# Kernel optimization log

Hardware: AMD Instinct MI355X
Metric: run time of the kernel (lower is better)

The kernel has to match this reference:

```python
import jax, jax.numpy as jnp
import numpy as np

N = 100000   # nodes
E = 1600000  # edges
B = 4096     # graphs
F_IN = 92
H = 51       # hidden_channels
ED = 10      # edge_dim
T = 7        # num_timesteps

def _p(key, shape, scale=0.1):
    return scale * jax.random.normal(key, shape, dtype=jnp.float32)

def setup_inputs():
    key = jax.random.key(0)
    ks = jax.random.split(key, 20)
    return {
        "x": jax.random.normal(ks[0], (N, F_IN), dtype=jnp.float32),
        "edge_index": jax.random.randint(ks[1], (2, E), 0, N),
        "edge_attr": jax.random.normal(ks[2], (E, ED), dtype=jnp.float32),
        "batch": jnp.sort(jax.random.randint(ks[3], (N,), 0, B)),
        "W1": _p(ks[4], (F_IN, H)), "b1": jnp.zeros((H,), jnp.float32),
        "We1": _p(ks[5], (H + ED, H)),
        "att_l": _p(ks[6], (H,)), "att_r": _p(ks[7], (H,)),
        "We2": _p(ks[8], (H, H)), "gate_bias": jnp.zeros((H,), jnp.float32),
        "Wih1": _p(ks[9], (H, 3 * H)), "bih1": jnp.zeros((3 * H,), jnp.float32),
        "Whh1": _p(ks[10], (H, 3 * H)), "bhh1": jnp.zeros((3 * H,), jnp.float32),
        "Wm": _p(ks[11], (H, H)),
        "att_src": _p(ks[12], (H,)), "att_dst": _p(ks[13], (H,)),
        "mol_bias": jnp.zeros((H,), jnp.float32),
        "Wih2": _p(ks[14], (H, 3 * H)), "bih2": jnp.zeros((3 * H,), jnp.float32),
        "Whh2": _p(ks[15], (H, 3 * H)), "bhh2": jnp.zeros((3 * H,), jnp.float32),
        "W2": _p(ks[16], (H, 1)), "b2": jnp.zeros((1,), jnp.float32),
    }

def _lrelu(v):
    return jax.nn.leaky_relu(v, 0.01)

def _seg_softmax(a, idx, num):
    # scatter-softmax over segments (PyG softmax with 1e-16 denom eps)
    m = jax.ops.segment_max(a, idx, num_segments=num)
    e = jnp.exp(a - m[idx])
    s = jax.ops.segment_sum(e, idx, num_segments=num)
    return e / (s[idx] + 1e-16)

def _gru(xin, h, Wih, bih, Whh, bhh):
    # torch.nn.GRUCell, gate order r, z, n
    gi = xin @ Wih + bih
    gh = h @ Whh + bhh
    ir, iz, inn = jnp.split(gi, 3, axis=-1)
    hr, hz, hn = jnp.split(gh, 3, axis=-1)
    r = jax.nn.sigmoid(ir + hr)
    z = jax.nn.sigmoid(iz + hz)
    n = jnp.tanh(inn + r * hn)
    return (1.0 - z) * n + z * h

def reference(x, edge_index, edge_attr, batch, W1, b1, We1, att_l, att_r, We2,
              gate_bias, Wih1, bih1, Whh1, bhh1, Wm, att_src, att_dst, mol_bias,
              Wih2, bih2, Whh2, bhh2, W2, b2):
    src, dst = edge_index[0], edge_index[1]
    # AttentiveFP.lin1 + leaky_relu
    x = _lrelu(x @ W1 + b1)                                        # (N, H)
    # GATEConv: edge-conditioned attention, aggregate to dst
    xe = _lrelu(jnp.concatenate([x[src], edge_attr], axis=-1) @ We1)  # (E, H)
    a = _lrelu(xe @ att_l + x[dst] @ att_r)                        # (E,)
    alpha = _seg_softmax(a, dst, N)
    h = jax.ops.segment_sum((xe @ We2) * alpha[:, None], dst, num_segments=N) + gate_bias
    h = jax.nn.elu(h)                                              # dropout off (eval)
    x = jax.nn.relu(_gru(h, x, Wih1, bih1, Whh1, bhh1))            # (N, H)
    # molecule readout: GATConv over bipartite (nodes -> graphs) edges (arange(N), batch)
    out = jax.nn.relu(jax.ops.segment_sum(x, batch, num_segments=B))  # (B, H)
    xl = x @ Wm                                                    # (N, H), constant over t
    al = xl @ att_src                                              # (N,)
    for _ in range(T):
        ar = (out @ Wm) @ att_dst                                  # (B,)
        a = _lrelu(al + ar[batch])
        alpha = _seg_softmax(a, batch, B)
        hm = jax.ops.segment_sum(xl * alpha[:, None], batch, num_segments=B) + mol_bias
        hm = jax.nn.elu(hm)
        out = jax.nn.relu(_gru(hm, out, Wih2, bih2, Whh2, bhh2))
    return out @ W2 + b2                                           # (B, 1)
```

## Files before the change

kernel.cpp:

```cpp
#include <hip/hip_runtime.h>
#include <stdint.h>

#define NN 100000
#define NE 1600000
#define NB 4096
#define FIN 92
#define H 51
#define H3 153
#define TSTEPS 7
#define SCAN_B 391
#define GG_BLOCKS 1024
#define GG_CHUNKS (NN / 32)

__device__ __align__(16) float g_x1[(size_t)NN * 52 + 64];
__device__ __align__(16) float g_p[(size_t)NN * 52 + 64];
__device__ float g_xr[NN];
__device__ float g_agg[(size_t)NN * H + 64];
__device__ float g_x2[(size_t)NN * H + 64];
__device__ float g_xl[(size_t)NN * H + 64];
__device__ float g_al[NN];
__device__ int   g_gs[NB + 2];
__device__ float g_wg1[H * H * 8];
__device__ float g_bg1[64 * 8];
__device__ float g_wg2[H * H * 8];
__device__ float g_bg2[64 * 8];
__device__ float g_wv[64];
__device__ int   g_cnt[NN];
__device__ int   g_rp[NN + 1];
__device__ int   g_cur[NN];
__device__ int   g_src[NE + 4];
__device__ __align__(16) float g_eac[(size_t)NE * 12 + 16];
__device__ int   g_bsum[512];
__device__ int   g_boff[512];

__device__ __forceinline__ float lrelu(float v) { return v > 0.f ? v : 0.01f * v; }
__device__ __forceinline__ float elu1(float v) { return v > 0.f ? v : expm1f(v); }
__device__ __forceinline__ float sigm(float v) { return 1.f / (1.f + __expf(-v)); }

__device__ __forceinline__ float bflo(uint32_t w) { union { uint32_t u; float f; } c; c.u = w << 16; return c.f; }
__device__ __forceinline__ float bfhi(uint32_t w) { union { uint32_t u; float f; } c; c.u = w & 0xffff0000u; return c.f; }
__device__ __forceinline__ uint32_t f2bf(float f) {
    uint32_t u = __float_as_uint(f);
    return (u + 0x7FFFu + ((u >> 16) & 1u)) >> 16;
}

__device__ __forceinline__ float wave_sum(float v) {
    v += __shfl_xor(v, 32, 64);
    v += __shfl_xor(v, 16, 64);
    v += __shfl_xor(v, 8, 64);
    v += __shfl_xor(v, 4, 64);
    v += __shfl_xor(v, 2, 64);
    v += __shfl_xor(v, 1, 64);
    return v;
}
__device__ __forceinline__ void wave_sum4(float& a, float& b, float& c, float& d) {
    a += __shfl_xor(a, 32, 64); b += __shfl_xor(b, 32, 64); c += __shfl_xor(c, 32, 64); d += __shfl_xor(d, 32, 64);
    a += __shfl_xor(a, 16, 64); b += __shfl_xor(b, 16, 64); c += __shfl_xor(c, 16, 64); d += __shfl_xor(d, 16, 64);
    a += __shfl_xor(a, 8, 64);  b += __shfl_xor(b, 8, 64);  c += __shfl_xor(c, 8, 64);  d += __shfl_xor(d, 8, 64);
    a += __shfl_xor(a, 4, 64);  b += __shfl_xor(b, 4, 64);  c += __shfl_xor(c, 4, 64);  d += __shfl_xor(d, 4, 64);
    a += __shfl_xor(a, 2, 64);  b += __shfl_xor(b, 2, 64);  c += __shfl_xor(c, 2, 64);  d += __shfl_xor(d, 2, 64);
    a += __shfl_xor(a, 1, 64);  b += __shfl_xor(b, 1, 64);  c += __shfl_xor(c, 1, 64);  d += __shfl_xor(d, 1, 64);
}

__device__ __forceinline__ float d4(float acc, float4 t, float4 wv) {
    return fmaf(t.x, wv.x, fmaf(t.y, wv.y, fmaf(t.z, wv.z, fmaf(t.w, wv.w, acc))));
}

__global__ __launch_bounds__(256) void k_init(const int* __restrict__ batch) {
    int n = blockIdx.x * 256 + threadIdx.x;
    if (n >= NN) return;
    g_cnt[n] = 0;
    int bn = batch[n];
    int bp = (n == 0) ? -1 : batch[n - 1];
    for (int b = bp + 1; b <= bn; ++b) g_gs[b] = n;
    if (n == NN - 1) for (int b = bn + 1; b <= NB; ++b) g_gs[b] = NN;
}

__global__ void k_prep(const float* __restrict__ Wih1, const float* __restrict__ bih1,
                       const float* __restrict__ Whh1, const float* __restrict__ bhh1,
                       const float* __restrict__ Wih2, const float* __restrict__ bih2,
                       const float* __restrict__ Whh2, const float* __restrict__ bhh2,
                       const float* __restrict__ Wm, const float* __restrict__ ad) {
    int id = blockIdx.x * 256 + threadIdx.x;
    int which = 0;
    const float *Wih, *bih, *Whh, *bhh;
    if (id < H * H) {
        which = 0; Wih = Wih1; bih = bih1; Whh = Whh1; bhh = bhh1;
    } else if (id < 2 * H * H) {
        which = 1; id -= H * H; Wih = Wih2; bih = bih2; Whh = Whh2; bhh = bhh2;
    } else {
        int k = id - 2 * H * H;
        if (k < 64) {
            float a = 0.f;
            if (k < H) for (int j = 0; j < H; ++j) a = fmaf(Wm[k * H + j], ad[j], a);
            g_wv[k] = a;
        }
        return;
    }
    float* Wg = which ? g_wg2 : g_wg1;
    float* bg = which ? g_bg2 : g_bg1;
    int k = id / H, j = id - k * H;
    float* o = Wg + (size_t)id * 8;
    o[0] = Wih[k * H3 + j];
    o[1] = Wih[k * H3 + H + j];
    o[2] = Wih[k * H3 + 2 * H + j];
    o[3] = Whh[k * H3 + j];
    o[4] = Whh[k * H3 + H + j];
    o[5] = Whh[k * H3 + 2 * H + j];
    o[6] = 0.f; o[7] = 0.f;
    if (id < H) {
        float* ob = bg + (size_t)id * 8;
        ob[0] = bih[id]; ob[1] = bih[H + id]; ob[2] = bih[2 * H + id];
        ob[3] = bhh[id]; ob[4] = bhh[H + id]; ob[5] = bhh[2 * H + id];
        ob[6] = 0.f; ob[7] = 0.f;
    }
}

__global__ __launch_bounds__(256) void k_count(const int* __restrict__ ei) {
    int e = blockIdx.x * 256 + threadIdx.x;
    if (e >= NE) return;
    atomicAdd(&g_cnt[ei[NE + e]], 1);
}

__global__ __launch_bounds__(256) void k_scan1() {
    __shared__ int sm[256];
    int tid = threadIdx.x;
    int i = blockIdx.x * 256 + tid;
    sm[tid] = (i < NN) ? g_cnt[i] : 0;
    __syncthreads();
#pragma unroll
    for (int off = 1; off < 256; off <<= 1) {
        int t = (tid >= off) ? sm[tid - off] : 0;
        __syncthreads();
        sm[tid] += t;
        __syncthreads();
    }
    if (i < NN) g_rp[i + 1] = sm[tid];
    if (tid == 255) g_bsum[blockIdx.x] = sm[255];
}

__global__ void k_scan2() {
    __shared__ int sm[512];
    int tid = threadIdx.x;
    sm[tid] = (tid < SCAN_B) ? g_bsum[tid] : 0;
    __syncthreads();
#pragma unroll
    for (int off = 1; off < 512; off <<= 1) {
        int t = (tid >= off) ? sm[tid - off] : 0;
        __syncthreads();
        sm[tid] += t;
        __syncthreads();
    }
    if (tid < SCAN_B) g_boff[tid] = (tid == 0) ? 0 : sm[tid - 1];
}

__global__ __launch_bounds__(256) void k_scan3() {
    int i = blockIdx.x * 256 + threadIdx.x;
    if (i >= NN) return;
    int v = g_rp[i + 1] + g_boff[blockIdx.x];
    g_rp[i + 1] = v;
    if (i == 0) { g_rp[0] = 0; g_cur[0] = 0; }
    if (i + 1 < NN) g_cur[i + 1] = v;
}

__global__ __launch_bounds__(256) void k_fill(const int* __restrict__ ei, const float* __restrict__ ea) {
    int e = blockIdx.x * 256 + threadIdx.x;
    if (e >= NE) return;
    int d = ei[NE + e];
    int pos = atomicAdd(&g_cur[d], 1);
    g_src[pos] = ei[e];
    const float2* s2 = (const float2*)(ea + (size_t)e * 10);
    float2 v0 = s2[0], v1 = s2[1], v2 = s2[2], v3 = s2[3], v4 = s2[4];
    float2* d2 = (float2*)(g_eac + (size_t)pos * 12);
    d2[0] = v0; d2[1] = v1; d2[2] = v2; d2[3] = v3; d2[4] = v4;
    d2[5] = make_float2(0.f, 0.f);
}

__global__ __launch_bounds__(256, 3) void k_lin1(const float* __restrict__ x, const float* __restrict__ W1,
                                                 const float* __restrict__ b1, const float* __restrict__ attr_,
                                                 const float* __restrict__ We1) {
    int n = blockIdx.x * 256 + threadIdx.x;
    if (n >= NN) return;
    const float4* xq4 = (const float4*)(x + (size_t)n * FIN);
    float acc[H];
#pragma unroll
    for (int h = 0; h < H; ++h) acc[h] = 0.f;
#pragma unroll 1
    for (int q = 0; q < FIN / 4; ++q) {
        float4 v = xq4[q];
        const float* wr = W1 + (4 * q) * H;
#pragma unroll
        for (int h = 0; h < H; ++h)
            acc[h] = fmaf(v.x, wr[h], fmaf(v.y, wr[H + h], fmaf(v.z, wr[2 * H + h], fmaf(v.w, wr[3 * H + h], acc[h]))));
    }
    float xrv = 0.f;
    float* xo = g_x1 + (size_t)n * 52;
#pragma unroll
    for (int h = 0; h < H; ++h) {
        float v = lrelu(acc[h] + b1[h]);
        acc[h] = v;
        xo[h] = v;
        xrv = fmaf(v, attr_[h], xrv);
    }
    xo[H] = 0.f;
    g_xr[n] = xrv;
    float* po = g_p + (size_t)n * 52;
#pragma unroll 1
    for (int h = 0; h < H; ++h) {
        float ph = 0.f;
#pragma unroll
        for (int k = 0; k < H; ++k) ph = fmaf(acc[k], We1[k * H + h], ph);
        po[h] = ph;
    }
    po[H] = 0.f;
}

#define MKE(q) make_float4( \
    (4*(q)+0) < 10 ? We1[(51 + 4*(q)+0) * H + lj] : 0.f, \
    (4*(q)+1) < 10 ? We1[(51 + 4*(q)+1) * H + lj] : 0.f, \
    (4*(q)+2) < 10 ? We1[(51 + 4*(q)+2) * H + lj] : 0.f, \
    (4*(q)+3) < 10 ? We1[(51 + 4*(q)+3) * H + lj] : 0.f)

__global__ __launch_bounds__(256, 4) void k_gate(const float* __restrict__ We1, const float* __restrict__ attl) {
    int lane = threadIdx.x & 63;
    int lj = lane < H ? lane : H - 1;
    int n = __builtin_amdgcn_readfirstlane(blockIdx.x * 4 + (threadIdx.x >> 6));
    float4 eq0 = MKE(0), eq1 = MKE(1), eq2 = MKE(2);
    float attlv = attl[lj];
    float xrd = g_xr[n];
    int rs = g_rp[n], re = g_rp[n + 1];
    float accH = 0.f, den = 0.f;
    int nb = (re - rs) >> 2;
    int idx = rs;
    float pv0 = 0.f, pv1 = 0.f, pv2 = 0.f, pv3 = 0.f;
    if (nb > 0) {
        int s0 = __builtin_amdgcn_readfirstlane(g_src[idx]);
        int s1 = __builtin_amdgcn_readfirstlane(g_src[idx + 1]);
        int s2 = __builtin_amdgcn_readfirstlane(g_src[idx + 2]);
        int s3 = __builtin_amdgcn_readfirstlane(g_src[idx + 3]);
        pv0 = g_p[(size_t)s0 * 52 + lane];
        pv1 = g_p[(size_t)s1 * 52 + lane];
        pv2 = g_p[(size_t)s2 * 52 + lane];
        pv3 = g_p[(size_t)s3 * 52 + lane];
    }
#pragma unroll 1
    for (int blk = 0; blk < nb; ++blk) {
        int ci = idx;
        float cp0 = pv0, cp1 = pv1, cp2 = pv2, cp3 = pv3;
        idx += 4;
        if (blk + 1 < nb) {
            int s0 = __builtin_amdgcn_readfirstlane(g_src[idx]);
            int s1 = __builtin_amdgcn_readfirstlane(g_src[idx + 1]);
            int s2 = __builtin_amdgcn_readfirstlane(g_src[idx + 2]);
            int s3 = __builtin_amdgcn_readfirstlane(g_src[idx + 3]);
            pv0 = g_p[(size_t)s0 * 52 + lane];
            pv1 = g_p[(size_t)s1 * 52 + lane];
            pv2 = g_p[(size_t)s2 * 52 + lane];
            pv3 = g_p[(size_t)s3 * 52 + lane];
        }
        const float4* ep0 = (const float4*)(g_eac + (size_t)ci * 12);
        const float4* ep1 = (const float4*)(g_eac + (size_t)(ci + 1) * 12);
        const float4* ep2 = (const float4*)(g_eac + (size_t)(ci + 2) * 12);
        const float4* ep3 = (const float4*)(g_eac + (size_t)(ci + 3) * 12);
        float xe0 = cp0, xe1 = cp1, xe2 = cp2, xe3 = cp3;
        xe0 = d4(xe0, ep0[0], eq0); xe0 = d4(xe0, ep0[1], eq1); xe0 = d4(xe0, ep0[2], eq2);
        xe1 = d4(xe1, ep1[0], eq0); xe1 = d4(xe1, ep1[1], eq1); xe1 = d4(xe1, ep1[2], eq2);
        xe2 = d4(xe2, ep2[0], eq0); xe2 = d4(xe2, ep2[1], eq1); xe2 = d4(xe2, ep2[2], eq2);
        xe3 = d4(xe3, ep3[0], eq0); xe3 = d4(xe3, ep3[1], eq1); xe3 = d4(xe3, ep3[2], eq2);
        float l0 = lrelu(xe0), l1 = lrelu(xe1), l2 = lrelu(xe2), l3 = lrelu(xe3);
        float p0 = (lane < H) ? l0 * attlv : 0.f;
        float p1 = (lane < H) ? l1 * attlv : 0.f;
        float p2 = (lane < H) ? l2 * attlv : 0.f;
        float p3 = (lane < H) ? l3 * attlv : 0.f;
        wave_sum4(p0, p1, p2, p3);
        float e0 = __expf(lrelu(p0 + xrd));
        float e1 = __expf(lrelu(p1 + xrd));
        float e2 = __expf(lrelu(p2 + xrd));
        float e3 = __expf(lrelu(p3 + xrd));
        accH = fmaf(e0, l0, accH); den += e0;
        accH = fmaf(e1, l1, accH); den += e1;
        accH = fmaf(e2, l2, accH); den += e2;
        accH = fmaf(e3, l3, accH); den += e3;
    }
    for (; idx < re; ++idx) {
        int s0 = __builtin_amdgcn_readfirstlane(g_src[idx]);
        float pvs = g_p[(size_t)s0 * 52 + lane];
        const float4* ep0 = (const float4*)(g_eac + (size_t)idx * 12);
        float xe0 = pvs;
        xe0 = d4(xe0, ep0[0], eq0); xe0 = d4(xe0, ep0[1], eq1); xe0 = d4(xe0, ep0[2], eq2);
        float l0 = lrelu(xe0);
        float a0 = wave_sum((lane < H) ? l0 * attlv : 0.f);
        float e0 = __expf(lrelu(a0 + xrd));
        accH = fmaf(e0, l0, accH); den += e0;
    }
    if (lane < H) g_agg[(size_t)n * H + lane] = accH / (den + 1e-16f);
}

__global__ __launch_bounds__(256) void k_gategru(const float* __restrict__ We2, const float* __restrict__ gb,
                                                 const float* __restrict__ Wm, const float* __restrict__ asrc) {
    __shared__ uint32_t wA[H * H];
    __shared__ uint32_t wB[H * H];
    __shared__ uint32_t wC[H * H];
    __shared__ float lbc[4][52][8];
    int tid = threadIdx.x;
    for (int i = tid; i < H * H; i += 256) {
        const float* s = g_wg1 + (size_t)i * 8;
        wA[i] = f2bf(s[0]) | (f2bf(s[1]) << 16);
        wB[i] = f2bf(s[2]) | (f2bf(s[3]) << 16);
        wC[i] = f2bf(s[4]) | (f2bf(s[5]) << 16);
    }
    __syncthreads();
    int w = tid >> 6;
    int lane = tid & 63;
    int lj = lane < H ? lane : H - 1;
    const float4* bp = (const float4*)(g_bg1 + lane * 8);
    float4 b0 = bp[0];
    float4 b1v = bp[1];
    float gbl = gb[lj];
    float asl = asrc[lj];
#pragma unroll 1
    for (int chunk = blockIdx.x; chunk < GG_CHUNKS; chunk += GG_BLOCKS) {
        int base = __builtin_amdgcn_readfirstlane(chunk * 32 + w * 8);
        float xj[8];
#pragma unroll
        for (int m = 0; m < 8; ++m) xj[m] = g_x1[(size_t)(base + m) * 52 + lane];
        float ac[8];
#pragma unroll
        for (int m = 0; m < 8; ++m) ac[m] = 0.f;
#pragma unroll 1
        for (int k = 0; k < H; ++k) {
            float wv = We2[k * H + lj];
#pragma unroll
            for (int m = 0; m < 8; ++m)
                ac[m] = fmaf(g_agg[(size_t)(base + m) * H + k], wv, ac[m]);
        }
        float hb[8];
#pragma unroll
        for (int m = 0; m < 8; ++m) hb[m] = elu1(ac[m] + gbl);
        if (lane < H) {
#pragma unroll
            for (int m = 0; m < 8; ++m) lbc[w][lane][m] = hb[m];
        }
        float gir[8], giz[8], gin[8], ghr[8], ghz[8], ghn[8];
#pragma unroll
        for (int m = 0; m < 8; ++m) { gir[m] = 0; giz[m] = 0; gin[m] = 0; ghr[m] = 0; ghz[m] = 0; ghn[m] = 0; }
#pragma unroll 1
        for (int k = 0; k < H; ++k) {
            uint32_t wa = wA[k * H + lj];
            uint32_t wb = wB[k * H + lj];
            uint32_t wc = wC[k * H + lj];
            float w0x = bflo(wa), w0y = bfhi(wa), w0z = bflo(wb);
            float w0w = bfhi(wb), w1x = bflo(wc), w1y = bfhi(wc);
            float4 h0 = *(const float4*)&lbc[w][k][0];
            float4 h1 = *(const float4*)&lbc[w][k][4];
            float hk[8] = { h0.x, h0.y, h0.z, h0.w, h1.x, h1.y, h1.z, h1.w };
#pragma unroll
            for (int m = 0; m < 8; ++m) {
                float xk = g_x1[(size_t)(base + m) * 52 + k];
                gir[m] = fmaf(hk[m], w0x, gir[m]); giz[m] = fmaf(hk[m], w0y, giz[m]); gin[m] = fmaf(hk[m], w0z, gin[m]);
                ghr[m] = fmaf(xk, w0w, ghr[m]);    ghz[m] = fmaf(xk, w1x, ghz[m]);    ghn[m] = fmaf(xk, w1y, ghn[m]);
            }
        }
        float o2[8];
#pragma unroll
        for (int m = 0; m < 8; ++m) {
            float r = sigm(gir[m] + b0.x + ghr[m] + b0.w);
            float z = sigm(giz[m] + b0.y + ghz[m] + b1v.x);
            float nn2 = tanhf(gin[m] + b0.z + r * (ghn[m] + b1v.y));
            o2[m] = fmaxf((1.f - z) * nn2 + z * xj[m], 0.f);
            if (lane < H) g_x2[(size_t)(base + m) * H + lane] = o2[m];
        }
        if (lane < H) {
#pragma unroll
            for (int m = 0; m < 8; ++m) lbc[w][lane][m] = o2[m];
        }
        float xl[8];
#pragma unroll
        for (int m = 0; m < 8; ++m) xl[m] = 0.f;
#pragma unroll 1
        for (int k = 0; k < H; ++k) {
            float wv = Wm[k * H + lj];
            float4 o0 = *(const float4*)&lbc[w][k][0];
            float4 o1 = *(const float4*)&lbc[w][k][4];
            xl[0] = fmaf(o0.x, wv, xl[0]); xl[1] = fmaf(o0.y, wv, xl[1]);
            xl[2] = fmaf(o0.z, wv, xl[2]); xl[3] = fmaf(o0.w, wv, xl[3]);
            xl[4] = fmaf(o1.x, wv, xl[4]); xl[5] = fmaf(o1.y, wv, xl[5]);
            xl[6] = fmaf(o1.z, wv, xl[6]); xl[7] = fmaf(o1.w, wv, xl[7]);
        }
        float v0, v1, v2, v3, v4, v5, v6, v7;
        v0 = (lane < H) ? xl[0] * asl : 0.f;
        v1 = (lane < H) ? xl[1] * asl : 0.f;
        v2 = (lane < H) ? xl[2] * asl : 0.f;
        v3 = (lane < H) ? xl[3] * asl : 0.f;
        v4 = (lane < H) ? xl[4] * asl : 0.f;
        v5 = (lane < H) ? xl[5] * asl : 0.f;
        v6 = (lane < H) ? xl[6] * asl : 0.f;
        v7 = (lane < H) ? xl[7] * asl : 0.f;
        wave_sum4(v0, v1, v2, v3);
        wave_sum4(v4, v5, v6, v7);
#pragma unroll
        for (int m = 0; m < 8; ++m)
            if (lane < H) g_xl[(size_t)(base + m) * H + lane] = xl[m];
        if (lane == 0) {
            g_al[base + 0] = v0; g_al[base + 1] = v1; g_al[base + 2] = v2; g_al[base + 3] = v3;
            g_al[base + 4] = v4; g_al[base + 5] = v5; g_al[base + 6] = v6; g_al[base + 7] = v7;
        }
    }
}

__global__ __launch_bounds__(256) void k_mol_all(const float* __restrict__ mb, const float* __restrict__ W2,
                                                 const float* __restrict__ b2, float* __restrict__ dout) {
    __shared__ uint32_t ldsWa[H * H];
    __shared__ uint32_t ldsWb[H * H];
    __shared__ uint32_t ldsWc[H * H];
    __shared__ float lbc[4][52][2];
    int tid = threadIdx.x;
    for (int i = tid; i < H * H; i += 256) {
        const float* s = g_wg2 + (size_t)i * 8;
        ldsWa[i] = f2bf(s[0]) | (f2bf(s[1]) << 16);
        ldsWb[i] = f2bf(s[2]) | (f2bf(s[3]) << 16);
        ldsWc[i] = f2bf(s[4]) | (f2bf(s[5]) << 16);
    }
    __syncthreads();
    int w = tid >> 6;
    int lane = tid & 63;
    int lj = lane < H ? lane : H - 1;
    int b = __builtin_amdgcn_readfirstlane(blockIdx.x * 4 + w);
    int gs = g_gs[b], ge = g_gs[b + 1];
    float oa = 0.f, ob = 0.f;
    int i = gs;
    for (; i + 2 <= ge; i += 2) {
        oa += g_x2[(size_t)i * H + lane];
        ob += g_x2[(size_t)(i + 1) * H + lane];
    }
    if (i < ge) oa += g_x2[(size_t)i * H + lane];
    float oj = fmaxf(oa + ob, 0.f);
    float wvl = g_wv[lane];
    float mbl = mb[lj];
    const float4* bp = (const float4*)(g_bg2 + lane * 8);
    float4 b0 = bp[0];
    float4 b1v = bp[1];
#pragma unroll 1
    for (int t = 0; t < TSTEPS; ++t) {
        float arb = wave_sum((lane < H) ? oj * wvl : 0.f);
        float sa = 0.f, sb = 0.f, aa = 0.f, ab = 0.f;
        i = gs;
        for (; i + 2 <= ge; i += 2) {
            float ev0 = __expf(lrelu(g_al[i] + arb));
            float ev1 = __expf(lrelu(g_al[i + 1] + arb));
            sa += ev0; sb += ev1;
            aa = fmaf(ev0, g_xl[(size_t)i * H + lane], aa);
            ab = fmaf(ev1, g_xl[(size_t)(i + 1) * H + lane], ab);
        }
        if (i < ge) {
            float ev0 = __expf(lrelu(g_al[i] + arb));
            sa += ev0;
            aa = fmaf(ev0, g_xl[(size_t)i * H + lane], aa);
        }
        float inv = 1.f / (sa + sb + 1e-16f);
        float hm = elu1((aa + ab) * inv + mbl);
        if (lane < H) { lbc[w][lane][0] = hm; lbc[w][lane][1] = oj; }
        float gir = 0, giz = 0, gin = 0, ghr = 0, ghz = 0, ghn = 0;
#pragma unroll 2
        for (int k = 0; k < H; ++k) {
            uint32_t wa = ldsWa[k * H + lj];
            uint32_t wb = ldsWb[k * H + lj];
            uint32_t wc = ldsWc[k * H + lj];
            float2 ho = *(const float2*)&lbc[w][k][0];
            float hmk = ho.x, ok = ho.y;
            gir = fmaf(hmk, bflo(wa), gir); giz = fmaf(hmk, bfhi(wa), giz); gin = fmaf(hmk, bflo(wb), gin);
            ghr = fmaf(ok, bfhi(wb), ghr);  ghz = fmaf(ok, bflo(wc), ghz);  ghn = fmaf(ok, bfhi(wc), ghn);
        }
        float r = sigm(gir + b0.x + ghr + b0.w);
        float z = sigm(giz + b0.y + ghz + b1v.x);
        float nn2 = tanhf(gin + b0.z + r * (ghn + b1v.y));
        oj = fmaxf((1.f - z) * nn2 + z * oj, 0.f);
    }
    float fv = wave_sum((lane < H) ? oj * W2[lj] : 0.f);
    if (lane == 0) dout[b] = fv + b2[0];
}

extern "C" void kernel_launch(void* const* d_in, const int* in_sizes, int n_in,
                              void* d_out, int out_size, void* d_ws, size_t ws_size,
                              hipStream_t stream) {
    const float* x     = (const float*)d_in[0];
    const int*   ei    = (const int*)d_in[1];
    const float* ea    = (const float*)d_in[2];
    const int*   batch = (const int*)d_in[3];
    const float* W1    = (const float*)d_in[4];
    const float* b1    = (const float*)d_in[5];
    const float* We1   = (const float*)d_in[6];
    const float* attl  = (const float*)d_in[7];
    const float* attr_ = (const float*)d_in[8];
    const float* We2   = (const float*)d_in[9];
    const float* gb    = (const float*)d_in[10];
    const float* Wm    = (const float*)d_in[15];
    const float* asrc  = (const float*)d_in[16];
    const float* adst  = (const float*)d_in[17];
    const float* mb    = (const float*)d_in[18];
    const float* W2    = (const float*)d_in[23];
    const float* b2    = (const float*)d_in[24];
    float* dout = (float*)d_out;

    k_init<<<SCAN_B, 256, 0, stream>>>(batch);
    k_count<<<NE / 256, 256, 0, stream>>>(ei);
    k_scan1<<<SCAN_B, 256, 0, stream>>>();
    k_scan2<<<1, 512, 0, stream>>>();
    k_scan3<<<SCAN_B, 256, 0, stream>>>();
    k_fill<<<NE / 256, 256, 0, stream>>>(ei, ea);

    k_prep<<<(2 * H * H + 64 + 255) / 256, 256, 0, stream>>>(
        (const float*)d_in[11], (const float*)d_in[12], (const float*)d_in[13], (const float*)d_in[14],
        (const float*)d_in[19], (const float*)d_in[20], (const float*)d_in[21], (const float*)d_in[22],
        Wm, adst);

    k_lin1<<<(NN + 255) / 256, 256, 0, stream>>>(x, W1, b1, attr_, We1);
    k_gate<<<NN / 4, 256, 0, stream>>>(We1, attl);
    k_gategru<<<GG_BLOCKS, 256, 0, stream>>>(We2, gb, Wm, asrc);
    k_mol_all<<<NB / 4, 256, 0, stream>>>(mb, W2, b2, dout);
}
```

Measured before the change: 659.4 us.

## Store gathered edge projections as bf16 and stage gategru inputs in shared memory

The per-node projection table g_p, gathered once per edge in k_gate, is now stored as bf16, which halves the bytes moved by the random gathers. In k_gategru the agg and x1 rows for each 8-node group are loaded with coalesced per-lane reads into shared-memory transposes. The inner k-loops then read them as float4 from LDS instead of issuing scalar global loads per k. The grid-stride block count also drops from 1024 to 768. The bf16 rounding of P adds precision error to the attention logits and messages, and the extra LDS arrays raise shared-memory use per block.

```diff
diff --git a/kernel.cpp b/kernel.cpp
--- a/kernel.cpp
+++ b/kernel.cpp
@@ -9,11 +9,11 @@
 #define H3 153
 #define TSTEPS 7
 #define SCAN_B 391
-#define GG_BLOCKS 1024
+#define GG_BLOCKS 768
 #define GG_CHUNKS (NN / 32)
 
 __device__ __align__(16) float g_x1[(size_t)NN * 52 + 64];
-__device__ __align__(16) float g_p[(size_t)NN * 52 + 64];
+__device__ __align__(16) unsigned short g_pb[(size_t)NN * 52 + 64];
 __device__ float g_xr[NN];
 __device__ float g_agg[(size_t)NN * H + 64];
 __device__ float g_x2[(size_t)NN * H + 64];
@@ -204,15 +204,15 @@
     }
     xo[H] = 0.f;
     g_xr[n] = xrv;
-    float* po = g_p + (size_t)n * 52;
+    unsigned short* po = g_pb + (size_t)n * 52;
 #pragma unroll 1
     for (int h = 0; h < H; ++h) {
         float ph = 0.f;
 #pragma unroll
         for (int k = 0; k < H; ++k) ph = fmaf(acc[k], We1[k * H + h], ph);
-        po[h] = ph;
-    }
-    po[H] = 0.f;
+        po[h] = (unsigned short)f2bf(ph);
+    }
+    po[H] = 0;
 }
 
 #define MKE(q) make_float4( \
@@ -238,10 +238,10 @@
         int s1 = __builtin_amdgcn_readfirstlane(g_src[idx + 1]);
         int s2 = __builtin_amdgcn_readfirstlane(g_src[idx + 2]);
         int s3 = __builtin_amdgcn_readfirstlane(g_src[idx + 3]);
-        pv0 = g_p[(size_t)s0 * 52 + lane];
-        pv1 = g_p[(size_t)s1 * 52 + lane];
-        pv2 = g_p[(size_t)s2 * 52 + lane];
-        pv3 = g_p[(size_t)s3 * 52 + lane];
+        pv0 = bflo(g_pb[(size_t)s0 * 52 + lane]);
+        pv1 = bflo(g_pb[(size_t)s1 * 52 + lane]);
+        pv2 = bflo(g_pb[(size_t)s2 * 52 + lane]);
+        pv3 = bflo(g_pb[(size_t)s3 * 52 + lane]);
     }
 #pragma unroll 1
     for (int blk = 0; blk < nb; ++blk) {
@@ -253,10 +253,10 @@
             int s1 = __builtin_amdgcn_readfirstlane(g_src[idx + 1]);
             int s2 = __builtin_amdgcn_readfirstlane(g_src[idx + 2]);
             int s3 = __builtin_amdgcn_readfirstlane(g_src[idx + 3]);
-            pv0 = g_p[(size_t)s0 * 52 + lane];
-            pv1 = g_p[(size_t)s1 * 52 + lane];
-            pv2 = g_p[(size_t)s2 * 52 + lane];
-            pv3 = g_p[(size_t)s3 * 52 + lane];
+            pv0 = bflo(g_pb[(size_t)s0 * 52 + lane]);
+            pv1 = bflo(g_pb[(size_t)s1 * 52 + lane]);
+            pv2 = bflo(g_pb[(size_t)s2 * 52 + lane]);
+            pv3 = bflo(g_pb[(size_t)s3 * 52 + lane]);
         }
         const float4* ep0 = (const float4*)(g_eac + (size_t)ci * 12);
         const float4* ep1 = (const float4*)(g_eac + (size_t)(ci + 1) * 12);
@@ -284,7 +284,7 @@
     }
     for (; idx < re; ++idx) {
         int s0 = __builtin_amdgcn_readfirstlane(g_src[idx]);
-        float pvs = g_p[(size_t)s0 * 52 + lane];
+        float pvs = bflo(g_pb[(size_t)s0 * 52 + lane]);
         const float4* ep0 = (const float4*)(g_eac + (size_t)idx * 12);
         float xe0 = pvs;
         xe0 = d4(xe0, ep0[0], eq0); xe0 = d4(xe0, ep0[1], eq1); xe0 = d4(xe0, ep0[2], eq2);
@@ -301,7 +301,9 @@
     __shared__ uint32_t wA[H * H];
     __shared__ uint32_t wB[H * H];
     __shared__ uint32_t wC[H * H];
-    __shared__ float lbc[4][52][8];
+    __shared__ float lA[4][52][8];
+    __shared__ float lX[4][52][8];
+    __shared__ float lH[4][52][8];
     int tid = threadIdx.x;
     for (int i = tid; i < H * H; i += 256) {
         const float* s = g_wg1 + (size_t)i * 8;
@@ -321,25 +323,35 @@
 #pragma unroll 1
     for (int chunk = blockIdx.x; chunk < GG_CHUNKS; chunk += GG_BLOCKS) {
         int base = __builtin_amdgcn_readfirstlane(chunk * 32 + w * 8);
-        float xj[8];
-#pragma unroll
-        for (int m = 0; m < 8; ++m) xj[m] = g_x1[(size_t)(base + m) * 52 + lane];
+        float xj[8], ag[8];
+#pragma unroll
+        for (int m = 0; m < 8; ++m) {
+            xj[m] = g_x1[(size_t)(base + m) * 52 + lane];
+            ag[m] = g_agg[(size_t)(base + m) * H + lane];
+        }
+        if (lane < H) {
+#pragma unroll
+            for (int m = 0; m < 8; ++m) { lA[w][lane][m] = ag[m]; lX[w][lane][m] = xj[m]; }
+        }
         float ac[8];
 #pragma unroll
         for (int m = 0; m < 8; ++m) ac[m] = 0.f;
 #pragma unroll 1
         for (int k = 0; k < H; ++k) {
             float wv = We2[k * H + lj];
-#pragma unroll
-            for (int m = 0; m < 8; ++m)
-                ac[m] = fmaf(g_agg[(size_t)(base + m) * H + k], wv, ac[m]);
+            float4 a0 = *(const float4*)&lA[w][k][0];
+            float4 a1 = *(const float4*)&lA[w][k][4];
+            ac[0] = fmaf(a0.x, wv, ac[0]); ac[1] = fmaf(a0.y, wv, ac[1]);
+            ac[2] = fmaf(a0.z, wv, ac[2]); ac[3] = fmaf(a0.w, wv, ac[3]);
+            ac[4] = fmaf(a1.x, wv, ac[4]); ac[5] = fmaf(a1.y, wv, ac[5]);
+            ac[6] = fmaf(a1.z, wv, ac[6]); ac[7] = fmaf(a1.w, wv, ac[7]);
         }
         float hb[8];
 #pragma unroll
         for (int m = 0; m < 8; ++m) hb[m] = elu1(ac[m] + gbl);
         if (lane < H) {
 #pragma unroll
-            for (int m = 0; m < 8; ++m) lbc[w][lane][m] = hb[m];
+            for (int m = 0; m < 8; ++m) lH[w][lane][m] = hb[m];
         }
         float gir[8], giz[8], gin[8], ghr[8], ghz[8], ghn[8];
 #pragma unroll
@@ -351,14 +363,16 @@
             uint32_t wc = wC[k * H + lj];
             float w0x = bflo(wa), w0y = bfhi(wa), w0z = bflo(wb);
             float w0w = bfhi(wb), w1x = bflo(wc), w1y = bfhi(wc);
-            float4 h0 = *(const float4*)&lbc[w][k][0];
-            float4 h1 = *(const float4*)&lbc[w][k][4];
+            float4 h0 = *(const float4*)&lH[w][k][0];
+            float4 h1 = *(const float4*)&lH[w][k][4];
+            float4 x0 = *(const float4*)&lX[w][k][0];
+            float4 x1v = *(const float4*)&lX[w][k][4];
             float hk[8] = { h0.x, h0.y, h0.z, h0.w, h1.x, h1.y, h1.z, h1.w };
+            float xk[8] = { x0.x, x0.y, x0.z, x0.w, x1v.x, x1v.y, x1v.z, x1v.w };
 #pragma unroll
             for (int m = 0; m < 8; ++m) {
-                float xk = g_x1[(size_t)(base + m) * 52 + k];
                 gir[m] = fmaf(hk[m], w0x, gir[m]); giz[m] = fmaf(hk[m], w0y, giz[m]); gin[m] = fmaf(hk[m], w0z, gin[m]);
-                ghr[m] = fmaf(xk, w0w, ghr[m]);    ghz[m] = fmaf(xk, w1x, ghz[m]);    ghn[m] = fmaf(xk, w1y, ghn[m]);
+                ghr[m] = fmaf(xk[m], w0w, ghr[m]); ghz[m] = fmaf(xk[m], w1x, ghz[m]); ghn[m] = fmaf(xk[m], w1y, ghn[m]);
             }
         }
         float o2[8];
@@ -372,7 +386,7 @@
         }
         if (lane < H) {
 #pragma unroll
-            for (int m = 0; m < 8; ++m) lbc[w][lane][m] = o2[m];
+            for (int m = 0; m < 8; ++m) lH[w][lane][m] = o2[m];
         }
         float xl[8];
 #pragma unroll
@@ -380,8 +394,8 @@
 #pragma unroll 1
         for (int k = 0; k < H; ++k) {
             float wv = Wm[k * H + lj];
-            float4 o0 = *(const float4*)&lbc[w][k][0];
-            float4 o1 = *(const float4*)&lbc[w][k][4];
+            float4 o0 = *(const float4*)&lH[w][k][0];
+            float4 o1 = *(const float4*)&lH[w][k][4];
             xl[0] = fmaf(o0.x, wv, xl[0]); xl[1] = fmaf(o0.y, wv, xl[1]);
             xl[2] = fmaf(o0.z, wv, xl[2]); xl[3] = fmaf(o0.w, wv, xl[3]);
             xl[4] = fmaf(o1.x, wv, xl[4]); xl[5] = fmaf(o1.y, wv, xl[5]);
```

New measurement: 656.8 us. About the same (-0.4%).
